# Kernel optimization log

Measured on AMD Instinct MI355X. Metric: run time of the kernel, lower is better.

The kernel has to match this reference:

```python
import jax, jax.numpy as jnp
import numpy as np


def setup_inputs() -> dict:
    key = jax.random.key(0)
    k1, k2 = jax.random.split(key)
    N = 8192
    means = jax.random.normal(k1, (N, 3), dtype=jnp.float32) * 2.0
    normals = jax.random.normal(k2, (N, 3), dtype=jnp.float32)
    normals = normals / (jnp.linalg.norm(normals, axis=-1, keepdims=True) + 1e-8)
    return {"means": means, "normals": normals, "k": 8}


def reference(means, normals, k):
    # Pairwise Euclidean distances via the ||a-b||^2 expansion: avoids the
    # N x N x 3 diff tensor the original torch code materializes (same math).
    sq = jnp.sum(means * means, axis=-1)                      # (N,)
    d2 = sq[:, None] + sq[None, :] - 2.0 * (means @ means.T)  # (N, N)
    dists = jnp.sqrt(jnp.maximum(d2, 0.0))
    # k+1 smallest distances (self is the 0-distance nearest); drop self.
    dists = jax.lax.stop_gradient(dists)
    _, idx = jax.lax.top_k(-dists, k + 1)                     # (N, k+1)
    idx = idx[:, 1:]                                          # (N, k)
    neighbors = means[idx]                                    # (N, k, 3)
    local_diff = neighbors - means[:, None, :]                # (N, k, 3)
    plane_dist = jnp.sum(local_diff * normals[:, None, :], axis=-1)  # (N, k)
    return jnp.mean(jnp.abs(plane_dist))
```

## Files before the change

kernel.cpp:

```cpp
#include <hip/hip_runtime.h>
#include <hip/hip_bf16.h>

#define NPTS 8192
#define KNN 8
#define RPB 16
#define STAGES 8
#define SCOLS 1024

typedef __attribute__((ext_vector_type(8))) short bf16x8;
typedef __attribute__((ext_vector_type(4))) float f32x4;

__device__ __forceinline__ unsigned int bf16rne(float v) {
    unsigned int u = __float_as_uint(v);
    return (u + 0x7FFFu + ((u >> 16) & 1u)) >> 16;
}
__device__ __forceinline__ float bf2f(unsigned int h) { return __uint_as_float(h << 16); }

__device__ __forceinline__ void insert8(unsigned int (&best)[KNN], unsigned int key) {
#pragma unroll
    for (int t = 0; t < KNN; ++t) {
        const unsigned int lo = min(best[t], key);
        key = max(best[t], key);
        best[t] = lo;
    }
}
__device__ __forceinline__ void insert4(unsigned int (&b)[4], unsigned int key) {
#pragma unroll
    for (int t = 0; t < 4; ++t) {
        const unsigned int lo = min(b[t], key);
        key = max(b[t], key);
        b[t] = lo;
    }
}

__global__ __launch_bounds__(512) void prep_thresh(const float* __restrict__ means,
                                                   float4* __restrict__ pts,
                                                   uint4* __restrict__ cf0,
                                                   uint4* __restrict__ cf1,
                                                   uint4* __restrict__ rf0,
                                                   uint4* __restrict__ rf1,
                                                   float* __restrict__ Tm_arr,
                                                   float* __restrict__ out) {
    __shared__ unsigned int lds4[16][32][5];
    __shared__ unsigned int lds8[4][32][8];
    const int tid = threadIdx.x;
    const int pl = tid & 31;
    const int cls = tid >> 5;
    const int pt = blockIdx.x * 32 + pl;
    if (blockIdx.x == 0 && tid == 0) out[0] = 0.0f;

    const float x = means[3 * pt + 0];
    const float y = means[3 * pt + 1];
    const float z = means[3 * pt + 2];
    const float sq = x * x + y * y + z * z;
    if (cls == 0) {
        pts[pt] = make_float4(x, y, z, sq);
        const unsigned int hx = bf16rne(x), lx = bf16rne(x - bf2f(hx));
        const unsigned int hy = bf16rne(y), ly = bf16rne(y - bf2f(hy));
        const unsigned int hz = bf16rne(z), lz = bf16rne(z - bf2f(hz));
        const unsigned int hs = bf16rne(sq), ls = bf16rne(sq - bf2f(hs));
        cf0[pt] = make_uint4(hx | (lx << 16), hx | (hy << 16),
                             ly | (hy << 16), hz | (lz << 16));
        cf1[pt] = make_uint4(hz | (hs << 16), ls | (0x3F80u << 16), 0x3F80u, 0u);
        const float ax = -2.0f * x, ay = -2.0f * y, az = -2.0f * z;
        const unsigned int hax = bf16rne(ax), lax = bf16rne(ax - bf2f(hax));
        const unsigned int hay = bf16rne(ay), lay = bf16rne(ay - bf2f(hay));
        const unsigned int haz = bf16rne(az), laz = bf16rne(az - bf2f(haz));
        const unsigned int hsr = bf16rne(sq), lsr = bf16rne(sq - bf2f(hsr));
        rf0[pt] = make_uint4(hax | (hax << 16), lax | (hay << 16),
                             hay | (lay << 16), haz | (haz << 16));
        rf1[pt] = make_uint4(laz | (0x3F80u << 16), 0x3F80u | (hsr << 16), lsr, 0u);
    }

    const float mx2 = -2.0f * x, my2 = -2.0f * y, mz2 = -2.0f * z;
    unsigned int b4[4] = {~0u, ~0u, ~0u, ~0u};
#pragma unroll 4
    for (int m = 0; m < 32; ++m) {
        const int col = 16 * (cls + 16 * m);
        const float qx = means[3 * col + 0];
        const float qy = means[3 * col + 1];
        const float qz = means[3 * col + 2];
        const float qsq = qx * qx + qy * qy + qz * qz;
        const float d2 = fmaxf(fmaf(mx2, qx, fmaf(my2, qy, fmaf(mz2, qz, sq + qsq))), 0.0f);
        unsigned int key = (__float_as_uint(d2) & 0xFFFFE000u) | (unsigned int)col;
        key = (col == pt) ? ~0u : key;
        insert4(b4, key);
    }
#pragma unroll
    for (int j = 0; j < 4; ++j) lds4[cls][pl][j] = b4[j];
    __syncthreads();
    if (tid < 128) {
        const int p2 = tid & 31, q = tid >> 5;
        unsigned int bb[KNN];
#pragma unroll
        for (int s = 0; s < KNN; ++s) bb[s] = ~0u;
        for (int c = q * 4; c < q * 4 + 4; ++c)
#pragma unroll
            for (int j = 0; j < 4; ++j) insert8(bb, lds4[c][p2][j]);
#pragma unroll
        for (int s = 0; s < KNN; ++s) lds8[q][p2][s] = bb[s];
    }
    __syncthreads();
    if (tid < 32) {
        unsigned int bb[KNN];
#pragma unroll
        for (int s = 0; s < KNN; ++s) bb[s] = ~0u;
        for (int q = 0; q < 4; ++q)
#pragma unroll
            for (int s = 0; s < KNN; ++s) insert8(bb, lds8[q][tid][s]);
        const float Tf = __uint_as_float(bb[7] & 0xFFFFE000u);
        Tm_arr[blockIdx.x * 32 + tid] = Tf + 0.02f + 2e-3f * Tf;
    }
}

__global__ __launch_bounds__(512) void mfma_knn(const uint4* __restrict__ cf0,
                                                const uint4* __restrict__ cf1,
                                                const uint4* __restrict__ rf0,
                                                const uint4* __restrict__ rf1,
                                                const float4* __restrict__ pts,
                                                const float* __restrict__ Tm_arr,
                                                const float* __restrict__ normals,
                                                float* __restrict__ out) {
    __shared__ unsigned int km[8][RPB][KNN + 1];
    const int tid = threadIdx.x;
    const int l = tid & 63;
    const int wv = __builtin_amdgcn_readfirstlane(tid >> 6);
    const int R = l & 15;
    const int g = l >> 4;
    const int arow = blockIdx.x * RPB + R;

    const float4 mp = pts[arow];
    const float ax = -2.0f * mp.x, ay = -2.0f * mp.y, az = -2.0f * mp.z;
    const float sq = mp.w;
    const float Tm = Tm_arr[arow];

    uint4 bu = make_uint4(0u, 0u, 0u, 0u);
    if (g == 0) bu = rf0[arow];
    else if (g == 1) bu = rf1[arow];
    union { uint4 u; bf16x8 v; } Bf; Bf.u = bu;
    const f32x4 zero = {0.0f, 0.0f, 0.0f, 0.0f};

    const uint4* __restrict__ asel = (g == 1) ? cf1 : cf0;

    unsigned int best[KNN];
#pragma unroll
    for (int s = 0; s < KNN; ++s) best[s] = ~0u;

#pragma unroll 1
    for (int s = 0; s < STAGES; ++s) {
        const int base = s * SCOLS + wv * 128;
        unsigned int m = 0u;
#pragma unroll
        for (int mt = 0; mt < 8; ++mt) {
            union { uint4 u; bf16x8 v; } Af;
            Af.u = asel[base + mt * 16 + R];
            const f32x4 acc = __builtin_amdgcn_mfma_f32_16x16x32_bf16(Af.v, Bf.v, zero, 0, 0, 0);
#pragma unroll
            for (int r = 0; r < 4; ++r) m = m + m + ((acc[r] <= Tm) ? 1u : 0u);
        }
        while (m) {
            const int b = __ffs(m) - 1;
            m &= m - 1;
            const int t = 31 - b;
            const int col = base + (t >> 2) * 16 + g * 4 + (t & 3);
            const float4 q = pts[col];
            const float d2 = fmaxf(fmaf(ax, q.x, fmaf(ay, q.y, fmaf(az, q.z, sq + q.w))), 0.0f);
            unsigned int key = (__float_as_uint(d2) & 0xFFFFE000u) | (unsigned int)col;
            key = (col == arow) ? ~0u : key;
            insert8(best, key);
        }
    }

#pragma unroll
    for (int st = 16; st <= 32; st <<= 1) {
        unsigned int tk[KNN];
#pragma unroll
        for (int s = 0; s < KNN; ++s) tk[s] = __shfl_xor(best[s], st);
#pragma unroll
        for (int s = 0; s < KNN; ++s) insert8(best, tk[s]);
    }
    if (l < RPB) {
#pragma unroll
        for (int s = 0; s < KNN; ++s) km[wv][l][s] = best[s];
    }
    for (int st = 1; st < 8; st <<= 1) {
        __syncthreads();
        if (((wv & (2 * st - 1)) == 0) && l < RPB) {
#pragma unroll
            for (int s = 0; s < KNN; ++s) insert8(best, km[wv + st][l][s]);
#pragma unroll
            for (int s = 0; s < KNN; ++s) km[wv][l][s] = best[s];
        }
    }

    if (wv == 0) {
        float sum = 0.0f;
        if (l < RPB) {
            const float nx = normals[3 * arow + 0];
            const float ny = normals[3 * arow + 1];
            const float nz = normals[3 * arow + 2];
#pragma unroll
            for (int s = 0; s < KNN; ++s) {
                const int nbr = (int)(best[s] & 0x1FFFu);
                const float4 q = pts[nbr];
                sum += fabsf((q.x - mp.x) * nx + (q.y - mp.y) * ny + (q.z - mp.z) * nz);
            }
        }
#pragma unroll
        for (int off = 8; off > 0; off >>= 1) sum += __shfl_down(sum, off);
        if (l == 0) atomicAdd(out, sum * (1.0f / ((float)NPTS * (float)KNN)));
    }
}

extern "C" void kernel_launch(void* const* d_in, const int* in_sizes, int n_in,
                              void* d_out, int out_size, void* d_ws, size_t ws_size,
                              hipStream_t stream) {
    const float* means = (const float*)d_in[0];
    const float* normals = (const float*)d_in[1];
    float* out = (float*)d_out;
    char* ws = (char*)d_ws;
    uint4* cf0 = (uint4*)ws;
    uint4* cf1 = (uint4*)(ws + 131072);
    uint4* rf0 = (uint4*)(ws + 262144);
    uint4* rf1 = (uint4*)(ws + 393216);
    float4* pts = (float4*)(ws + 524288);
    float* Tm = (float*)(ws + 655360);

    prep_thresh<<<NPTS / 32, 512, 0, stream>>>(means, pts, cf0, cf1, rf0, rf1, Tm, out);
    mfma_knn<<<NPTS / RPB, 512, 0, stream>>>(cf0, cf1, rf0, rf1, pts, Tm, normals, out);
}
```

Baseline: 35.02 us.

## Double waves per block to 16, halving columns per wave in kNN scan

The kNN kernel now launches 1024 threads (16 waves) per block instead of 512, so each wave scans 64 columns per stage instead of 128. The four A-fragment loads are issued up front and skipped for the unused lane groups, and the candidate bitmask shrinks to 16 bits. The goal is more parallelism and latency hiding, with shorter per-wave candidate-insertion loops. In exchange, the cross-wave LDS merge tree gains an extra level, and register pressure under launch bounds of 1024 with 2 blocks may limit occupancy.

Result: slower. 41.43 us (+18.3%).

```diff
diff --git a/kernel.cpp b/kernel.cpp
--- a/kernel.cpp
+++ b/kernel.cpp
@@ -4,6 +4,8 @@
 #define NPTS 8192
 #define KNN 8
 #define RPB 16
+#define THREADS 1024
+#define NWAVES 16
 #define STAGES 8
 #define SCOLS 1024
 
@@ -113,15 +115,15 @@
     }
 }
 
-__global__ __launch_bounds__(512) void mfma_knn(const uint4* __restrict__ cf0,
-                                                const uint4* __restrict__ cf1,
-                                                const uint4* __restrict__ rf0,
-                                                const uint4* __restrict__ rf1,
-                                                const float4* __restrict__ pts,
-                                                const float* __restrict__ Tm_arr,
-                                                const float* __restrict__ normals,
-                                                float* __restrict__ out) {
-    __shared__ unsigned int km[8][RPB][KNN + 1];
+__global__ __launch_bounds__(THREADS, 2) void mfma_knn(const uint4* __restrict__ cf0,
+                                                       const uint4* __restrict__ cf1,
+                                                       const uint4* __restrict__ rf0,
+                                                       const uint4* __restrict__ rf1,
+                                                       const float4* __restrict__ pts,
+                                                       const float* __restrict__ Tm_arr,
+                                                       const float* __restrict__ normals,
+                                                       float* __restrict__ out) {
+    __shared__ unsigned int km[NWAVES][RPB][KNN + 1];
     const int tid = threadIdx.x;
     const int l = tid & 63;
     const int wv = __builtin_amdgcn_readfirstlane(tid >> 6);
@@ -141,6 +143,7 @@
     const f32x4 zero = {0.0f, 0.0f, 0.0f, 0.0f};
 
     const uint4* __restrict__ asel = (g == 1) ? cf1 : cf0;
+    const int lofs = wv * 64 + R;
 
     unsigned int best[KNN];
 #pragma unroll
@@ -148,21 +151,59 @@
 
 #pragma unroll 1
     for (int s = 0; s < STAGES; ++s) {
-        const int base = s * SCOLS + wv * 128;
-        unsigned int m = 0u;
-#pragma unroll
-        for (int mt = 0; mt < 8; ++mt) {
-            union { uint4 u; bf16x8 v; } Af;
-            Af.u = asel[base + mt * 16 + R];
-            const f32x4 acc = __builtin_amdgcn_mfma_f32_16x16x32_bf16(Af.v, Bf.v, zero, 0, 0, 0);
-#pragma unroll
-            for (int r = 0; r < 4; ++r) m = m + m + ((acc[r] <= Tm) ? 1u : 0u);
-        }
+        const int base = s * SCOLS + lofs;
+        uint4 a0 = {}, a1 = {}, a2 = {}, a3 = {};
+        if (g < 2) {
+            a0 = asel[base + 0];
+            a1 = asel[base + 16];
+            a2 = asel[base + 32];
+            a3 = asel[base + 48];
+        }
+        unsigned int n0, n1, n2, n3;
+        {
+            union { uint4 u; bf16x8 v; } Af;
+            Af.u = a0;
+            const f32x4 acc = __builtin_amdgcn_mfma_f32_16x16x32_bf16(Af.v, Bf.v, zero, 0, 0, 0);
+            n0 = (acc[0] <= Tm) ? 1u : 0u;
+            n0 = n0 + n0 + ((acc[1] <= Tm) ? 1u : 0u);
+            n0 = n0 + n0 + ((acc[2] <= Tm) ? 1u : 0u);
+            n0 = n0 + n0 + ((acc[3] <= Tm) ? 1u : 0u);
+        }
+        {
+            union { uint4 u; bf16x8 v; } Af;
+            Af.u = a1;
+            const f32x4 acc = __builtin_amdgcn_mfma_f32_16x16x32_bf16(Af.v, Bf.v, zero, 0, 0, 0);
+            n1 = (acc[0] <= Tm) ? 1u : 0u;
+            n1 = n1 + n1 + ((acc[1] <= Tm) ? 1u : 0u);
+            n1 = n1 + n1 + ((acc[2] <= Tm) ? 1u : 0u);
+            n1 = n1 + n1 + ((acc[3] <= Tm) ? 1u : 0u);
+        }
+        {
+            union { uint4 u; bf16x8 v; } Af;
+            Af.u = a2;
+            const f32x4 acc = __builtin_amdgcn_mfma_f32_16x16x32_bf16(Af.v, Bf.v, zero, 0, 0, 0);
+            n2 = (acc[0] <= Tm) ? 1u : 0u;
+            n2 = n2 + n2 + ((acc[1] <= Tm) ? 1u : 0u);
+            n2 = n2 + n2 + ((acc[2] <= Tm) ? 1u : 0u);
+            n2 = n2 + n2 + ((acc[3] <= Tm) ? 1u : 0u);
+        }
+        {
+            union { uint4 u; bf16x8 v; } Af;
+            Af.u = a3;
+            const f32x4 acc = __builtin_amdgcn_mfma_f32_16x16x32_bf16(Af.v, Bf.v, zero, 0, 0, 0);
+            n3 = (acc[0] <= Tm) ? 1u : 0u;
+            n3 = n3 + n3 + ((acc[1] <= Tm) ? 1u : 0u);
+            n3 = n3 + n3 + ((acc[2] <= Tm) ? 1u : 0u);
+            n3 = n3 + n3 + ((acc[3] <= Tm) ? 1u : 0u);
+        }
+        unsigned int m = (n0 << 12) | (n1 << 8) | (n2 << 4) | n3;
+
+        const int base_c = s * SCOLS + wv * 64;
         while (m) {
             const int b = __ffs(m) - 1;
             m &= m - 1;
-            const int t = 31 - b;
-            const int col = base + (t >> 2) * 16 + g * 4 + (t & 3);
+            const int t = 15 - b;
+            const int col = base_c + (t >> 2) * 16 + g * 4 + (t & 3);
             const float4 q = pts[col];
             const float d2 = fmaxf(fmaf(ax, q.x, fmaf(ay, q.y, fmaf(az, q.z, sq + q.w))), 0.0f);
             unsigned int key = (__float_as_uint(d2) & 0xFFFFE000u) | (unsigned int)col;
@@ -183,7 +224,7 @@
 #pragma unroll
         for (int s = 0; s < KNN; ++s) km[wv][l][s] = best[s];
     }
-    for (int st = 1; st < 8; st <<= 1) {
+    for (int st = 1; st < NWAVES; st <<= 1) {
         __syncthreads();
         if (((wv & (2 * st - 1)) == 0) && l < RPB) {
 #pragma unroll
@@ -227,5 +268,5 @@
     float* Tm = (float*)(ws + 655360);
 
     prep_thresh<<<NPTS / 32, 512, 0, stream>>>(means, pts, cf0, cf1, rf0, rf1, Tm, out);
-    mfma_knn<<<NPTS / RPB, 512, 0, stream>>>(cf0, cf1, rf0, rf1, pts, Tm, normals, out);
-}
+    mfma_knn<<<NPTS / RPB, THREADS, 0, stream>>>(cf0, cf1, rf0, rf1, pts, Tm, normals, out);
+}
```
